# Kernel tuning notes

Measured on AMD Instinct MI355X. Metric: run time of the kernel, lower is better.

## Reference

```python
import jax, jax.numpy as jnp
import numpy as np

B, T, M, D, H, DK, DV = 2, 1024, 1024, 1024, 16, 64, 64
R = 2 * T + M  # number of relative positions required by rel_shift path


def setup_inputs() -> dict:
    key = jax.random.key(0)
    ks = jax.random.split(key, 11)
    s = 0.02
    return {
        "inputs": jax.random.normal(ks[0], (B, T, D), jnp.float32),
        "attention_mask": jnp.ones((B, T, M + T), jnp.float32),
        "positional_encodings": jax.random.normal(ks[1], (R, D), jnp.float32),
        "memory": jax.random.normal(ks[2], (B, M, D), jnp.float32),
        "Wq": jax.random.normal(ks[3], (D, H * DK), jnp.float32) * s,
        "Wk": jax.random.normal(ks[4], (D, H * DK), jnp.float32) * s,
        "Wv": jax.random.normal(ks[5], (D, H * DV), jnp.float32) * s,
        "Wr": jax.random.normal(ks[6], (D, H * DK), jnp.float32) * s,
        "r_w_bias": jax.random.normal(ks[7], (H, DK), jnp.float32) * s,
        "r_r_bias": jax.random.normal(ks[8], (H, DK), jnp.float32) * s,
        "W_out": jax.random.normal(ks[9], (H * DV, D), jnp.float32) * s,
    }


def _rel_shift(m, attention_length):
    # m: [T_q, T_q + L] -> [T_q, L], TXL relative shift via reshape/slice
    tq, total = m.shape
    x = m.reshape(total, tq)[1:].reshape(tq, total - 1)
    return x[:, :attention_length]


def reference(inputs, attention_mask, positional_encodings, memory,
              Wq, Wk, Wv, Wr, r_w_bias, r_r_bias, W_out):
    b, t, d = inputs.shape
    values = jnp.concatenate([memory, inputs], axis=1)  # [B, L, D]
    L = values.shape[1]
    q = (inputs @ Wq).reshape(b, t, H, DK)
    k = (values @ Wk).reshape(b, L, H, DK)
    v = (values @ Wv).reshape(b, L, H, DV)
    rk = (positional_encodings @ Wr).reshape(-1, H, DK)  # [R, H, DK]
    # content + relative logits (TXL)
    content = jnp.einsum('bthd,bThd->bhtT', q + r_w_bias, k)        # [B,H,T,L]
    rel = jnp.einsum('bthd,rhd->bhtr', q + r_r_bias, rk)            # [B,H,T,R]
    rel = jax.vmap(jax.vmap(lambda m: _rel_shift(m, L)))(rel)       # [B,H,T,L]
    logits = (content + rel) * (DK ** -0.5)
    masked = logits - (1.0 - attention_mask[:, None, :, :]) * 1e30
    w = jax.nn.softmax(masked, axis=-1)
    attn = jnp.einsum('bhtT,bThd->bthd', w, v)                      # [B,T,H,DV]
    return attn.reshape(b, t, H * DV) @ W_out
```

## Files before the change

kernel.cpp:

```cpp
#include <hip/hip_runtime.h>
#include <hip/hip_fp16.h>
#include <stdint.h>

#define Bz 2
#define Tq 1024
#define Mm 1024
#define Hh 16
#define Ll 2048
#define Rr 3072

typedef __attribute__((ext_vector_type(8))) short bf16x8;
typedef __attribute__((ext_vector_type(4))) float f32x4;

typedef __attribute__((address_space(3))) uint8_t lds_u8_t;
typedef __attribute__((address_space(1))) uint8_t glb_u8_t;

__device__ __forceinline__ void gl2lds16(const void* g, void* l) {
  __builtin_amdgcn_global_load_lds((const glb_u8_t*)g, (lds_u8_t*)l, 16, 0, 0);
}

__device__ __forceinline__ unsigned short f2bf(float f) {
  unsigned int u = __builtin_bit_cast(unsigned int, f);
  u = u + 0x7fffu + ((u >> 16) & 1u);
  return (unsigned short)(u >> 16);
}
__device__ __forceinline__ float b2f(unsigned short s) {
  unsigned int u = ((unsigned int)s) << 16;
  return __builtin_bit_cast(float, u);
}

__global__ __launch_bounds__(256) void k_prep2(
    const float* __restrict__ x, const float* __restrict__ mem,
    const float* __restrict__ pos, const float* __restrict__ mask,
    const float* __restrict__ w0, const float* __restrict__ w1,
    const float* __restrict__ w2, const float* __restrict__ w3,
    const float* __restrict__ w4,
    unsigned short* __restrict__ vin, unsigned short* __restrict__ pb,
    unsigned short* __restrict__ mb,
    unsigned short* __restrict__ t0, unsigned short* __restrict__ t1,
    unsigned short* __restrict__ t2, unsigned short* __restrict__ t3,
    unsigned short* __restrict__ t4) {
  __shared__ float tile[64][65];
  int bid = blockIdx.x;
  if (bid < 4096) {
    int idx = bid * 256 + threadIdx.x;
    int e = idx << 2;
    int row = e >> 10, col = e & 1023;
    int b = row >> 11, l = row & 2047;
    const float* s = (l < Mm) ? (mem + (((size_t)b * Mm + l) << 10) + col)
                              : (x + (((size_t)b * Tq + (l - Mm)) << 10) + col);
    float4 v = *(const float4*)s;
    ushort4 o;
    o.x = f2bf(v.x); o.y = f2bf(v.y); o.z = f2bf(v.z); o.w = f2bf(v.w);
    *(ushort4*)(vin + e) = o;
  } else if (bid < 7168) {
    int idx = (bid - 4096) * 256 + threadIdx.x;
    int e = idx << 2;
    float4 v = *(const float4*)(pos + e);
    ushort4 t;
    t.x = f2bf(v.x); t.y = f2bf(v.y); t.z = f2bf(v.z); t.w = f2bf(v.w);
    *(ushort4*)(pb + e) = t;
  } else if (bid < 11264) {
    int idx = (bid - 7168) * 256 + threadIdx.x;
    int e = idx << 2;
    const float BIGM = 1.442695e30f;
    float4 v = *(const float4*)(mask + e);
    ushort4 t;
    t.x = f2bf((1.0f - v.x) * BIGM); t.y = f2bf((1.0f - v.y) * BIGM);
    t.z = f2bf((1.0f - v.z) * BIGM); t.w = f2bf((1.0f - v.w) * BIGM);
    *(ushort4*)(mb + e) = t;
  } else {
    int r3 = bid - 11264;
    int mz = r3 >> 8, rem = r3 & 255;
    const float* W;
    unsigned short* WT;
    switch (mz) {
      case 0: W = w0; WT = t0; break;
      case 1: W = w1; WT = t1; break;
      case 2: W = w2; WT = t2; break;
      case 3: W = w3; WT = t3; break;
      default: W = w4; WT = t4; break;
    }
    int k0 = (rem >> 4) * 64, n0 = (rem & 15) * 64;
    int tid = threadIdx.x;
    int rr = tid >> 4, c4 = (tid & 15) * 4;
#pragma unroll
    for (int it = 0; it < 4; ++it) {
      int r = rr + it * 16;
      float4 v = *(const float4*)(W + (size_t)(k0 + r) * 1024 + n0 + c4);
      tile[r][c4] = v.x; tile[r][c4 + 1] = v.y;
      tile[r][c4 + 2] = v.z; tile[r][c4 + 3] = v.w;
    }
    __syncthreads();
#pragma unroll
    for (int it = 0; it < 4; ++it) {
      int n = rr + it * 16;
      ushort4 o;
      o.x = f2bf(tile[c4 + 0][n]); o.y = f2bf(tile[c4 + 1][n]);
      o.z = f2bf(tile[c4 + 2][n]); o.w = f2bf(tile[c4 + 3][n]);
      *(ushort4*)(WT + (size_t)(n0 + n) * 1024 + k0 + c4) = o;
    }
  }
}

template <int RMAP>
__device__ __forceinline__ void gemm_pipe(const unsigned short* __restrict__ A,
                                          const unsigned short* __restrict__ Bt,
                                          int m0, int n0, unsigned short* As,
                                          unsigned short* Bs, f32x4 acc[4][4]) {
  const int tid = threadIdx.x;
  const int w = tid >> 6, lane = tid & 63;
  const int quad = lane >> 4, li = lane & 15;
  const int wr = w >> 1, wc = w & 1;
  f32x4 z = {0.f, 0.f, 0.f, 0.f};
#pragma unroll
  for (int mi = 0; mi < 4; ++mi)
#pragma unroll
    for (int ni = 0; ni < 4; ++ni) acc[mi][ni] = z;

  const int rs = lane >> 2;
  const int cs = lane & 3;

#pragma unroll
  for (int s = 0; s < 2; ++s) {
    int i = w * 2 + s;
    int r = i * 16 + rs;
    int c = cs ^ ((r >> 1) & 3);
    int ar = m0 + r;
    if (RMAP) ar = ar + 1024 + (ar & 1024);
    gl2lds16(A + (size_t)ar * 1024 + c * 8, (char*)As + i * 1024);
    gl2lds16(Bt + (size_t)(n0 + r) * 1024 + c * 8, (char*)Bs + i * 1024);
  }

  for (int k0 = 0; k0 < 1024; k0 += 32) {
    const int bo = ((k0 >> 5) & 1) * 8192;
    const int no = bo ^ 8192;
    __builtin_amdgcn_s_waitcnt(0x0F70);
    __syncthreads();
    if (k0 + 32 < 1024) {
#pragma unroll
      for (int s = 0; s < 2; ++s) {
        int i = w * 2 + s;
        int r = i * 16 + rs;
        int c = cs ^ ((r >> 1) & 3);
        int ar = m0 + r;
        if (RMAP) ar = ar + 1024 + (ar & 1024);
        gl2lds16(A + (size_t)ar * 1024 + k0 + 32 + c * 8,
                 (char*)As + no + i * 1024);
        gl2lds16(Bt + (size_t)(n0 + r) * 1024 + k0 + 32 + c * 8,
                 (char*)Bs + no + i * 1024);
      }
    }
    bf16x8 af[4], bfr[4];
#pragma unroll
    for (int mi = 0; mi < 4; ++mi) {
      int r = wr * 64 + mi * 16 + li;
      int ch = quad ^ ((r >> 1) & 3);
      af[mi] = *(const bf16x8*)((const char*)As + bo + r * 64 + ch * 16);
    }
#pragma unroll
    for (int ni = 0; ni < 4; ++ni) {
      int r = wc * 64 + ni * 16 + li;
      int ch = quad ^ ((r >> 1) & 3);
      bfr[ni] = *(const bf16x8*)((const char*)Bs + bo + r * 64 + ch * 16);
    }
#pragma unroll
    for (int mi = 0; mi < 4; ++mi)
#pragma unroll
      for (int ni = 0; ni < 4; ++ni)
        acc[mi][ni] = __builtin_amdgcn_mfma_f32_16x16x32_bf16(
            af[mi], bfr[ni], acc[mi][ni], 0, 0, 0);
  }
}

__global__ __launch_bounds__(256) void k_proj(
    const unsigned short* __restrict__ Vin, const unsigned short* __restrict__ Pb,
    const unsigned short* __restrict__ WqT, const unsigned short* __restrict__ WkT,
    const unsigned short* __restrict__ WvT, const unsigned short* __restrict__ WrT,
    unsigned short* __restrict__ qb, unsigned short* __restrict__ kb,
    unsigned short* __restrict__ vtb, unsigned short* __restrict__ rkb) {
  __shared__ unsigned short As[2 * 128 * 32];
  __shared__ unsigned short Bs[2 * 128 * 32];
  const int t = blockIdx.x;
  const int tid = threadIdx.x, w = tid >> 6, lane = tid & 63;
  const int quad = lane >> 4, li = lane & 15, wr = w >> 1, wc = w & 1;
  f32x4 acc[4][4];

  if (t < 256) {
    int m0 = (t >> 3) * 128, n0 = (t & 7) * 128;
    gemm_pipe<0>(Vin, WkT, m0, n0, As, Bs, acc);
#pragma unroll
    for (int mi = 0; mi < 4; ++mi)
#pragma unroll
      for (int ni = 0; ni < 4; ++ni)
#pragma unroll
        for (int reg = 0; reg < 4; ++reg) {
          int rrow = m0 + wr * 64 + mi * 16 + quad * 4 + reg;
          int cc = n0 + wc * 64 + ni * 16 + li;
          kb[(size_t)rrow * 1024 + cc] = f2bf(acc[mi][ni][reg]);
        }
  } else if (t < 512) {
    int tt = t - 256;
    int m0 = (tt >> 3) * 128, n0 = (tt & 7) * 128;
    gemm_pipe<0>(Vin, WvT, m0, n0, As, Bs, acc);
#pragma unroll
    for (int mi = 0; mi < 4; ++mi)
#pragma unroll
      for (int ni = 0; ni < 4; ++ni) {
        int r0 = m0 + wr * 64 + mi * 16 + quad * 4;
        int b = r0 >> 11, l0 = r0 & 2047;
        int cc = n0 + wc * 64 + ni * 16 + li;
        ushort4 o;
        o.x = f2bf(acc[mi][ni][0]); o.y = f2bf(acc[mi][ni][1]);
        o.z = f2bf(acc[mi][ni][2]); o.w = f2bf(acc[mi][ni][3]);
        *(ushort4*)(vtb + ((size_t)(b * 1024 + cc)) * Ll + l0) = o;
      }
  } else if (t < 640) {
    int tt = t - 512;
    int m0 = (tt >> 3) * 128, n0 = (tt & 7) * 128;
    gemm_pipe<1>(Vin, WqT, m0, n0, As, Bs, acc);
#pragma unroll
    for (int mi = 0; mi < 4; ++mi)
#pragma unroll
      for (int ni = 0; ni < 4; ++ni)
#pragma unroll
        for (int reg = 0; reg < 4; ++reg) {
          int rrow = m0 + wr * 64 + mi * 16 + quad * 4 + reg;
          int cc = n0 + wc * 64 + ni * 16 + li;
          qb[(size_t)rrow * 1024 + cc] = f2bf(acc[mi][ni][reg]);
        }
  } else {
    int tt = t - 640;
    int m0 = (tt >> 3) * 128, n0 = (tt & 7) * 128;
    gemm_pipe<0>(Pb, WrT, m0, n0, As, Bs, acc);
#pragma unroll
    for (int mi = 0; mi < 4; ++mi)
#pragma unroll
      for (int ni = 0; ni < 4; ++ni)
#pragma unroll
        for (int reg = 0; reg < 4; ++reg) {
          int rrow = m0 + wr * 64 + mi * 16 + quad * 4 + reg;
          int cc = n0 + wc * 64 + ni * 16 + li;
          rkb[(size_t)rrow * 1024 + cc] = f2bf(acc[mi][ni][reg]);
        }
  }
}

__global__ __launch_bounds__(256) void k_gemm_out64(
    const unsigned short* __restrict__ attnb, const unsigned short* __restrict__ WoT,
    float* __restrict__ out) {
  __shared__ unsigned short As[2 * 64 * 32];
  __shared__ unsigned short Bs[2 * 128 * 32];
  int m0 = blockIdx.x * 64, n0 = blockIdx.y * 128;
  const int tid = threadIdx.x, w = tid >> 6, lane = tid & 63;
  const int quad = lane >> 4, li = lane & 15, wr = w >> 1, wc = w & 1;
  f32x4 z = {0.f, 0.f, 0.f, 0.f};
  f32x4 acc[2][4];
#pragma unroll
  for (int mi = 0; mi < 2; ++mi)
#pragma unroll
    for (int ni = 0; ni < 4; ++ni) acc[mi][ni] = z;
  const int rs = lane >> 2, cs = lane & 3;

  {
    int r = w * 16 + rs;
    int c = cs ^ ((r >> 1) & 3);
    gl2lds16(attnb + (size_t)(m0 + r) * 1024 + c * 8, (char*)As + w * 1024);
  }
#pragma unroll
  for (int s = 0; s < 2; ++s) {
    int i = w * 2 + s;
    int r = i * 16 + rs;
    int c = cs ^ ((r >> 1) & 3);
    gl2lds16(WoT + (size_t)(n0 + r) * 1024 + c * 8, (char*)Bs + i * 1024);
  }

  for (int k0 = 0; k0 < 1024; k0 += 32) {
    const int boa = ((k0 >> 5) & 1) * 4096;
    const int bob = ((k0 >> 5) & 1) * 8192;
    __builtin_amdgcn_s_waitcnt(0x0F70);
    __syncthreads();
    if (k0 + 32 < 1024) {
      {
        int r = w * 16 + rs;
        int c = cs ^ ((r >> 1) & 3);
        gl2lds16(attnb + (size_t)(m0 + r) * 1024 + k0 + 32 + c * 8,
                 (char*)As + (boa ^ 4096) + w * 1024);
      }
#pragma unroll
      for (int s = 0; s < 2; ++s) {
        int i = w * 2 + s;
        int r = i * 16 + rs;
        int c = cs ^ ((r >> 1) & 3);
        gl2lds16(WoT + (size_t)(n0 + r) * 1024 + k0 + 32 + c * 8,
                 (char*)Bs + (bob ^ 8192) + i * 1024);
      }
    }
    bf16x8 af[2], bfr[4];
#pragma unroll
    for (int mi = 0; mi < 2; ++mi) {
      int r = wr * 32 + mi * 16 + li;
      int ch = quad ^ ((r >> 1) & 3);
      af[mi] = *(const bf16x8*)((const char*)As + boa + r * 64 + ch * 16);
    }
#pragma unroll
    for (int ni = 0; ni < 4; ++ni) {
      int r = wc * 64 + ni * 16 + li;
      int ch = quad ^ ((r >> 1) & 3);
      bfr[ni] = *(const bf16x8*)((const char*)Bs + bob + r * 64 + ch * 16);
    }
#pragma unroll
    for (int mi = 0; mi < 2; ++mi)
#pragma unroll
      for (int ni = 0; ni < 4; ++ni)
        acc[mi][ni] = __builtin_amdgcn_mfma_f32_16x16x32_bf16(
            af[mi], bfr[ni], acc[mi][ni], 0, 0, 0);
  }
#pragma unroll
  for (int mi = 0; mi < 2; ++mi)
#pragma unroll
    for (int ni = 0; ni < 4; ++ni)
#pragma unroll
      for (int reg = 0; reg < 4; ++reg) {
        int rrow = m0 + wr * 32 + mi * 16 + quad * 4 + reg;
        int cc = n0 + wc * 64 + ni * 16 + li;
        out[(size_t)rrow * 1024 + cc] = acc[mi][ni][reg];
      }
}

__global__ __launch_bounds__(256, 2) void k_attn(
    const unsigned short* __restrict__ qb, const float* __restrict__ rwb,
    const float* __restrict__ rrb,
    const unsigned short* __restrict__ kb, const unsigned short* __restrict__ vt,
    const unsigned short* __restrict__ rkb, const unsigned short* __restrict__ mb,
    unsigned short* __restrict__ attnb) {
  __shared__ unsigned short Ks[2][64 * 64];
  __shared__ unsigned short Vs[2][64 * 64];
  __shared__ unsigned short Rs[256 * 64];
  __shared__ unsigned short Sb[4][16 * 72];

  const int tid = threadIdx.x;
  const int w = tid >> 6, lane = tid & 63;
  const int quad = lane >> 4, li = lane & 15;
  const int qt = blockIdx.x, h = blockIdx.y, b = blockIdx.z;
  const int t0blk = qt * 64;
  const int t0w = t0blk + w * 16;
  const int rboff = 48 - 16 * w;
  const int rbase0 = Tq - t0blk - 63;

  bf16x8 aqw[2], aqr[2];
  {
    const unsigned short* p1 = qb + ((size_t)((b * Tq + t0w + li) * Hh + h)) * 64;
#pragma unroll
    for (int ks = 0; ks < 2; ++ks) {
      bf16x8 qf = *(const bf16x8*)(p1 + ks * 32 + quad * 8);
      const float* wp = rwb + h * 64 + ks * 32 + quad * 8;
      const float* rp = rrb + h * 64 + ks * 32 + quad * 8;
      float4 w0 = *(const float4*)wp, w1 = *(const float4*)(wp + 4);
      float4 r0 = *(const float4*)rp, r1 = *(const float4*)(rp + 4);
      float wv[8] = {w0.x, w0.y, w0.z, w0.w, w1.x, w1.y, w1.z, w1.w};
      float rv[8] = {r0.x, r0.y, r0.z, r0.w, r1.x, r1.y, r1.z, r1.w};
#pragma unroll
      for (int i2 = 0; i2 < 8; ++i2) {
        float qv = b2f((unsigned short)qf[i2]);
        aqw[ks][i2] = (short)f2bf(qv + wv[i2]);
        aqr[ks][i2] = (short)f2bf(qv + rv[i2]);
      }
    }
  }

  f32x4 z = {0.f, 0.f, 0.f, 0.f};
  f32x4 o[4];
  o[0] = z; o[1] = z; o[2] = z; o[3] = z;
  f32x4 ol = z;

  const int srow = lane >> 3;
  const int scs = lane & 7;
  const float SC = 0.125f * 1.4426950408889634f;
  const short oneb = 0x3F80;
  const bf16x8 onesf = {oneb, oneb, oneb, oneb, oneb, oneb, oneb, oneb};

  unsigned short* pw = &Sb[w][0];
  const unsigned short* mrowA = mb + ((size_t)(b * Tq + t0w + li)) * Ll;
  int srcl[4];
#pragma unroll
  for (int reg = 0; reg < 4; ++reg) {
    int row = quad * 4 + reg;
    srcl[reg] = (lane & 48) + ((li + row + 1) & 15);
  }

#pragma unroll
  for (int s = 0; s < 4; ++s) {
    int i = w * 4 + s;
    int r = i * 8 + srow;
    int gr = rbase0 + r;
    if (gr > Rr - 1) gr = Rr - 1;
    int c = scs ^ (r & 7);
    gl2lds16(rkb + ((size_t)gr * Hh + h) * 64 + c * 8, (char*)Rs + i * 1024);
  }
#pragma unroll
  for (int s = 0; s < 2; ++s) {
    int i = w * 2 + s;
    int r = i * 8 + srow;
    int c = scs ^ (r & 7);
    gl2lds16(kb + ((size_t)((b * Ll + r) * Hh + h)) * 64 + c * 8,
             (char*)Ks[0] + i * 1024);
    gl2lds16(vt + ((size_t)((b * Hh + h) * 64 + r)) * Ll + c * 8,
             (char*)Vs[0] + i * 1024);
  }
  bf16x8 nmv0 = *(const bf16x8*)(mrowA + quad * 8);
  bf16x8 nmv1 = *(const bf16x8*)(mrowA + 32 + quad * 8);

  for (int jt = 0; jt < 32; ++jt) {
    const int j0 = jt * 64;
    const int cur = jt & 1, nxt = cur ^ 1;
    __builtin_amdgcn_s_waitcnt(0x0F70);
    __syncthreads();
    bf16x8 mv0 = nmv0, mv1 = nmv1;
    if (jt < 31) {
      const int j0n = j0 + 64;
#pragma unroll
      for (int s = 0; s < 2; ++s) {
        int i = w * 2 + s;
        int r = i * 8 + srow;
        int c = scs ^ (r & 7);
        gl2lds16(kb + ((size_t)((b * Ll + j0n + r) * Hh + h)) * 64 + c * 8,
                 (char*)Ks[nxt] + i * 1024);
        gl2lds16(vt + ((size_t)((b * Hh + h) * 64 + r)) * Ll + j0n + c * 8,
                 (char*)Vs[nxt] + i * 1024);
      }
#pragma unroll
      for (int s = 0; s < 2; ++s) {
        int i2 = w * 2 + s;
        int rr = i2 * 8 + srow;
        int ofs = j0 + 128 + rr;
        int gr = rbase0 + ofs;
        if (gr > Rr - 1) gr = Rr - 1;
        int ring = ofs & 255;
        int c = scs ^ (rr & 7);
        gl2lds16(rkb + ((size_t)gr * Hh + h) * 64 + c * 8, (char*)Rs + ring * 128);
      }
      nmv0 = *(const bf16x8*)(mrowA + j0n + quad * 8);
      nmv1 = *(const bf16x8*)(mrowA + j0n + 32 + quad * 8);
    }
    asm volatile("" ::: "memory");
    const unsigned short* KsC = Ks[cur];
    const unsigned short* VsC = Vs[cur];
    f32x4 sc[4];
    sc[0] = z; sc[1] = z; sc[2] = z; sc[3] = z;
    __builtin_amdgcn_s_setprio(1);
#pragma unroll
    for (int ks = 0; ks < 2; ++ks)
#pragma unroll
      for (int nt = 0; nt < 4; ++nt) {
        int j = nt * 16 + li;
        int ch = (ks * 4 + quad) ^ (j & 7);
        bf16x8 kf = *(const bf16x8*)((const char*)KsC + j * 128 + ch * 16);
        sc[nt] = __builtin_amdgcn_mfma_f32_16x16x32_bf16(aqw[ks], kf, sc[nt], 0, 0, 0);
      }
    f32x4 bd[5];
    bd[0] = z; bd[1] = z; bd[2] = z; bd[3] = z; bd[4] = z;
#pragma unroll
    for (int ks = 0; ks < 2; ++ks)
#pragma unroll
      for (int nt = 0; nt < 5; ++nt) {
        int pr = (rboff + nt * 16 + li + j0) & 255;
        int ch = (ks * 4 + quad) ^ (pr & 7);
        bf16x8 rf = *(const bf16x8*)((const char*)Rs + pr * 128 + ch * 16);
        bd[nt] = __builtin_amdgcn_mfma_f32_16x16x32_bf16(aqr[ks], rf, bd[nt], 0, 0, 0);
      }
    __builtin_amdgcn_s_setprio(0);
    float rot[4][4];
#pragma unroll
    for (int nt = 0; nt < 4; ++nt)
#pragma unroll
      for (int reg = 0; reg < 4; ++reg)
        rot[nt][reg] = __shfl(sc[nt][reg], srcl[reg], 64);
#pragma unroll
    for (int nt = 0; nt < 5; ++nt)
#pragma unroll
      for (int reg = 0; reg < 4; ++reg) {
        int row = quad * 4 + reg;
        int jj = nt * 16 + li + row - 15;
        int ntlo = (nt == 0) ? 3 : (nt - 1);
        int nthi = (nt > 3) ? 0 : nt;
        float val = ((li + row) >= 15) ? rot[nthi][reg] : rot[ntlo][reg];
        float s = val + bd[nt][reg];
        if ((unsigned)jj < 64u)
          pw[row * 72 + jj] = __builtin_bit_cast(unsigned short, __float2half(s));
      }
    __builtin_amdgcn_s_waitcnt(0xc07f);
    bf16x8 apv[2];
#pragma unroll
    for (int ks = 0; ks < 2; ++ks) {
      const int cofs = ks * 32 + quad * 8;
      ushort4 s0 = *(const ushort4*)(pw + li * 72 + cofs);
      ushort4 s1 = *(const ushort4*)(pw + li * 72 + cofs + 4);
      bf16x8 mv = ks ? mv1 : mv0;
      unsigned short su[8] = {s0.x, s0.y, s0.z, s0.w, s1.x, s1.y, s1.z, s1.w};
#pragma unroll
      for (int i2 = 0; i2 < 8; ++i2) {
        float sf = __half2float(__builtin_bit_cast(__half, su[i2]));
        float mvf = b2f((unsigned short)mv[i2]);
        float p = exp2f(sf * SC - mvf);
        apv[ks][i2] = (short)f2bf(p);
      }
    }
    __builtin_amdgcn_s_setprio(1);
#pragma unroll
    for (int ks = 0; ks < 2; ++ks)
      ol = __builtin_amdgcn_mfma_f32_16x16x32_bf16(apv[ks], onesf, ol, 0, 0, 0);
#pragma unroll
    for (int ks = 0; ks < 2; ++ks)
#pragma unroll
      for (int nt = 0; nt < 4; ++nt) {
        int dv = nt * 16 + li;
        int ch = (ks * 4 + quad) ^ (dv & 7);
        bf16x8 vf = *(const bf16x8*)((const char*)VsC + dv * 128 + ch * 16);
        o[nt] = __builtin_amdgcn_mfma_f32_16x16x32_bf16(apv[ks], vf, o[nt], 0, 0, 0);
      }
    __builtin_amdgcn_s_setprio(0);
  }
  float inv[4];
#pragma unroll
  for (int reg = 0; reg < 4; ++reg) inv[reg] = 1.0f / ol[reg];
#pragma unroll
  for (int nt = 0; nt < 4; ++nt)
#pragma unroll
    for (int reg = 0; reg < 4; ++reg) {
      int trow = t0w + quad * 4 + reg;
      attnb[((size_t)(b * Tq + trow)) * 1024 + h * 64 + nt * 16 + li] =
          f2bf(o[nt][reg] * inv[reg]);
    }
}

extern "C" void kernel_launch(void* const* d_in, const int* in_sizes, int n_in,
                              void* d_out, int out_size, void* d_ws, size_t ws_size,
                              hipStream_t stream) {
  const float* x = (const float*)d_in[0];
  const float* mask = (const float*)d_in[1];
  const float* pos = (const float*)d_in[2];
  const float* mem = (const float*)d_in[3];
  const float* Wq = (const float*)d_in[4];
  const float* Wk = (const float*)d_in[5];
  const float* Wv = (const float*)d_in[6];
  const float* Wr = (const float*)d_in[7];
  const float* rwb = (const float*)d_in[8];
  const float* rrb = (const float*)d_in[9];
  const float* Wo = (const float*)d_in[10];
  float* out = (float*)d_out;

  uint8_t* ws = (uint8_t*)d_ws;
  const size_t MB = 1024 * 1024;
  unsigned short* Vinb = (unsigned short*)(ws + 0);
  unsigned short* WqT = (unsigned short*)(ws + 8 * MB);
  unsigned short* WkT = (unsigned short*)(ws + 10 * MB);
  unsigned short* WvT = (unsigned short*)(ws + 12 * MB);
  unsigned short* WrT = (unsigned short*)(ws + 14 * MB);
  unsigned short* WoT = (unsigned short*)(ws + 16 * MB);
  unsigned short* Pb = (unsigned short*)(ws + 18 * MB);
  unsigned short* qb = (unsigned short*)(ws + 24 * MB);
  unsigned short* kb = (unsigned short*)(ws + 32 * MB);
  unsigned short* vtb = (unsigned short*)(ws + 40 * MB);
  unsigned short* rkb = (unsigned short*)(ws + 48 * MB);
  unsigned short* mbb = (unsigned short*)(ws + 54 * MB);
  unsigned short* attnb = (unsigned short*)(ws + 19 * MB);

  hipLaunchKernelGGL(k_prep2, dim3(12544), dim3(256), 0, stream,
                     x, mem, pos, mask, Wq, Wk, Wv, Wr, Wo,
                     Vinb, Pb, mbb, WqT, WkT, WvT, WrT, WoT);
  hipLaunchKernelGGL(k_proj, dim3(832), dim3(256), 0, stream,
                     Vinb, Pb, WqT, WkT, WvT, WrT, qb, kb, vtb, rkb);
  hipLaunchKernelGGL(k_attn, dim3(16, 16, 2), dim3(256), 0, stream,
                     qb, rwb, rrb, kb, vtb, rkb, mbb, attnb);
  hipLaunchKernelGGL(k_gemm_out64, dim3(32, 8), dim3(256), 0, stream,
                     attnb, WoT, out);
}
```

Before: 255.8 us.

## Software-pipeline attention loop so PV of previous tile overlaps current QK/rel MFMAs

Restructures the attention main loop so that the softmax-exponent and P·V step for tile jt-1 runs after the QK and relative-position MFMAs of tile jt, with V loads issued one iteration later and a drain step after the loop. It also remaps the block index so that consecutive blocks share the same query tile across different heads and batches, which is meant to improve L2 reuse of the mask and relative-key rows. The aim is to hide LDS write/read latency of the score buffer and overlap the exp work with matrix work. In exchange there is more register pressure from keeping scores live across iterations, and the ordering of writes and reads on the per-wave score buffer becomes more delicate.

```diff
diff --git a/kernel.cpp b/kernel.cpp
--- a/kernel.cpp
+++ b/kernel.cpp
@@ -342,7 +342,10 @@
   const int tid = threadIdx.x;
   const int w = tid >> 6, lane = tid & 63;
   const int quad = lane >> 4, li = lane & 15;
-  const int qt = blockIdx.x, h = blockIdx.y, b = blockIdx.z;
+  const int flat = blockIdx.x + 16 * blockIdx.y + 256 * blockIdx.z;
+  const int qt = (flat >> 3) & 15;
+  const int g = 4 * (flat & 7) + (flat >> 7);
+  const int h = g & 15, b = g >> 4;
   const int t0blk = qt * 64;
   const int t0w = t0blk + w * 16;
   const int rboff = 48 - 16 * w;
@@ -389,6 +392,39 @@
     srcl[reg] = (lane & 48) + ((li + row + 1) & 15);
   }
 
+  auto finish = [&](const unsigned short* VsP, bf16x8 mvF0, bf16x8 mvF1) {
+    bf16x8 apv[2];
+#pragma unroll
+    for (int ks = 0; ks < 2; ++ks) {
+      const int cofs = ks * 32 + quad * 8;
+      ushort4 s0 = *(const ushort4*)(pw + li * 72 + cofs);
+      ushort4 s1 = *(const ushort4*)(pw + li * 72 + cofs + 4);
+      bf16x8 mv = ks ? mvF1 : mvF0;
+      unsigned short su[8] = {s0.x, s0.y, s0.z, s0.w, s1.x, s1.y, s1.z, s1.w};
+#pragma unroll
+      for (int i2 = 0; i2 < 8; ++i2) {
+        float sf = __half2float(__builtin_bit_cast(__half, su[i2]));
+        float mvf = b2f((unsigned short)mv[i2]);
+        float p = exp2f(sf * SC - mvf);
+        apv[ks][i2] = (short)f2bf(p);
+      }
+    }
+    __builtin_amdgcn_s_setprio(1);
+#pragma unroll
+    for (int ks = 0; ks < 2; ++ks)
+      ol = __builtin_amdgcn_mfma_f32_16x16x32_bf16(apv[ks], onesf, ol, 0, 0, 0);
+#pragma unroll
+    for (int ks = 0; ks < 2; ++ks)
+#pragma unroll
+      for (int nt = 0; nt < 4; ++nt) {
+        int dv = nt * 16 + li;
+        int ch = (ks * 4 + quad) ^ (dv & 7);
+        bf16x8 vf = *(const bf16x8*)((const char*)VsP + dv * 128 + ch * 16);
+        o[nt] = __builtin_amdgcn_mfma_f32_16x16x32_bf16(apv[ks], vf, o[nt], 0, 0, 0);
+      }
+    __builtin_amdgcn_s_setprio(0);
+  };
+
 #pragma unroll
   for (int s = 0; s < 4; ++s) {
     int i = w * 4 + s;
@@ -405,18 +441,15 @@
     int c = scs ^ (r & 7);
     gl2lds16(kb + ((size_t)((b * Ll + r) * Hh + h)) * 64 + c * 8,
              (char*)Ks[0] + i * 1024);
-    gl2lds16(vt + ((size_t)((b * Hh + h) * 64 + r)) * Ll + c * 8,
-             (char*)Vs[0] + i * 1024);
-  }
-  bf16x8 nmv0 = *(const bf16x8*)(mrowA + quad * 8);
-  bf16x8 nmv1 = *(const bf16x8*)(mrowA + 32 + quad * 8);
+  }
+  bf16x8 nmv0 = {0, 0, 0, 0, 0, 0, 0, 0};
+  bf16x8 nmv1 = {0, 0, 0, 0, 0, 0, 0, 0};
 
   for (int jt = 0; jt < 32; ++jt) {
     const int j0 = jt * 64;
-    const int cur = jt & 1, nxt = cur ^ 1;
     __builtin_amdgcn_s_waitcnt(0x0F70);
     __syncthreads();
-    bf16x8 mv0 = nmv0, mv1 = nmv1;
+    bf16x8 mvF0 = nmv0, mvF1 = nmv1;
     if (jt < 31) {
       const int j0n = j0 + 64;
 #pragma unroll
@@ -425,9 +458,7 @@
         int r = i * 8 + srow;
         int c = scs ^ (r & 7);
         gl2lds16(kb + ((size_t)((b * Ll + j0n + r) * Hh + h)) * 64 + c * 8,
-                 (char*)Ks[nxt] + i * 1024);
-        gl2lds16(vt + ((size_t)((b * Hh + h) * 64 + r)) * Ll + j0n + c * 8,
-                 (char*)Vs[nxt] + i * 1024);
+                 (char*)Ks[(jt + 1) & 1] + i * 1024);
       }
 #pragma unroll
       for (int s = 0; s < 2; ++s) {
@@ -440,12 +471,19 @@
         int c = scs ^ (rr & 7);
         gl2lds16(rkb + ((size_t)gr * Hh + h) * 64 + c * 8, (char*)Rs + ring * 128);
       }
-      nmv0 = *(const bf16x8*)(mrowA + j0n + quad * 8);
-      nmv1 = *(const bf16x8*)(mrowA + j0n + 32 + quad * 8);
-    }
+    }
+#pragma unroll
+    for (int s = 0; s < 2; ++s) {
+      int i = w * 2 + s;
+      int r = i * 8 + srow;
+      int c = scs ^ (r & 7);
+      gl2lds16(vt + ((size_t)((b * Hh + h) * 64 + r)) * Ll + j0 + c * 8,
+               (char*)Vs[jt & 1] + i * 1024);
+    }
+    nmv0 = *(const bf16x8*)(mrowA + j0 + quad * 8);
+    nmv1 = *(const bf16x8*)(mrowA + j0 + 32 + quad * 8);
     asm volatile("" ::: "memory");
-    const unsigned short* KsC = Ks[cur];
-    const unsigned short* VsC = Vs[cur];
+    const unsigned short* KsC = Ks[jt & 1];
     f32x4 sc[4];
     sc[0] = z; sc[1] = z; sc[2] = z; sc[3] = z;
     __builtin_amdgcn_s_setprio(1);
@@ -470,6 +508,7 @@
         bd[nt] = __builtin_amdgcn_mfma_f32_16x16x32_bf16(aqr[ks], rf, bd[nt], 0, 0, 0);
       }
     __builtin_amdgcn_s_setprio(0);
+    if (jt > 0) finish(Vs[(jt - 1) & 1], mvF0, mvF1);
     float rot[4][4];
 #pragma unroll
     for (int nt = 0; nt < 4; ++nt)
@@ -489,38 +528,11 @@
         if ((unsigned)jj < 64u)
           pw[row * 72 + jj] = __builtin_bit_cast(unsigned short, __float2half(s));
       }
-    __builtin_amdgcn_s_waitcnt(0xc07f);
-    bf16x8 apv[2];
-#pragma unroll
-    for (int ks = 0; ks < 2; ++ks) {
-      const int cofs = ks * 32 + quad * 8;
-      ushort4 s0 = *(const ushort4*)(pw + li * 72 + cofs);
-      ushort4 s1 = *(const ushort4*)(pw + li * 72 + cofs + 4);
-      bf16x8 mv = ks ? mv1 : mv0;
-      unsigned short su[8] = {s0.x, s0.y, s0.z, s0.w, s1.x, s1.y, s1.z, s1.w};
-#pragma unroll
-      for (int i2 = 0; i2 < 8; ++i2) {
-        float sf = __half2float(__builtin_bit_cast(__half, su[i2]));
-        float mvf = b2f((unsigned short)mv[i2]);
-        float p = exp2f(sf * SC - mvf);
-        apv[ks][i2] = (short)f2bf(p);
-      }
-    }
-    __builtin_amdgcn_s_setprio(1);
-#pragma unroll
-    for (int ks = 0; ks < 2; ++ks)
-      ol = __builtin_amdgcn_mfma_f32_16x16x32_bf16(apv[ks], onesf, ol, 0, 0, 0);
-#pragma unroll
-    for (int ks = 0; ks < 2; ++ks)
-#pragma unroll
-      for (int nt = 0; nt < 4; ++nt) {
-        int dv = nt * 16 + li;
-        int ch = (ks * 4 + quad) ^ (dv & 7);
-        bf16x8 vf = *(const bf16x8*)((const char*)VsC + dv * 128 + ch * 16);
-        o[nt] = __builtin_amdgcn_mfma_f32_16x16x32_bf16(apv[ks], vf, o[nt], 0, 0, 0);
-      }
-    __builtin_amdgcn_s_setprio(0);
-  }
+  }
+  __builtin_amdgcn_s_waitcnt(0x0F70);
+  __syncthreads();
+  finish(Vs[1], nmv0, nmv1);
+
   float inv[4];
 #pragma unroll
   for (int reg = 0; reg < 4; ++reg) inv[reg] = 1.0f / ol[reg];
```

New measurement: 253.2 us. About the same (-1.0%).
